# Kernel tuning notes

Measured on AMD Instinct MI355X. Metric: run time of the kernel, lower is better.

Reference implementation:

```python
import jax, jax.numpy as jnp
import numpy as np

TOKEN_SIZE = 4
NEIGHBOR_SIZE = 3


def setup_inputs() -> dict:
    key = jax.random.key(0)
    ks = jax.random.split(key, 8)
    B, C, H, W = 8, 256, 64, 64
    return {
        "blue_feat": jax.random.normal(ks[0], (B, C, H, W), jnp.float32),
        "white_feat": jax.random.normal(ks[1], (B, C, H, W), jnp.float32),
        "Wq": jax.random.normal(ks[2], (C, C), jnp.float32) * 0.05,
        "bq": jax.random.normal(ks[3], (C,), jnp.float32) * 0.05,
        "Wk": jax.random.normal(ks[4], (C, C), jnp.float32) * 0.05,
        "bk": jax.random.normal(ks[5], (C,), jnp.float32) * 0.05,
        "Wv": jax.random.normal(ks[6], (C, C), jnp.float32) * 0.05,
        "bv": jax.random.normal(ks[7], (C,), jnp.float32) * 0.05,
    }


def _tokens(x, nh, nw, ts):
    # [B,C,H,W] -> [B,nh,nw,C,ts*ts]
    B, C = x.shape[0], x.shape[1]
    return (x.reshape(B, C, nh, ts, nw, ts)
             .transpose(0, 2, 4, 1, 3, 5)
             .reshape(B, nh, nw, C, ts * ts))


def reference(blue_feat, white_feat, Wq, bq, Wk, bk, Wv, bv):
    ts, ns = TOKEN_SIZE, NEIGHBOR_SIZE
    pad = ns // 2
    B, C, H, W = blue_feat.shape
    scale = float((ts * ts) ** -0.5)

    # 1x1 conv projections (pointwise channel mix + bias)
    Q = jnp.einsum('bchw,oc->bohw', blue_feat, Wq) + bq[None, :, None, None]
    K = jnp.einsum('bchw,oc->bohw', white_feat, Wk) + bk[None, :, None, None]
    V = jnp.einsum('bchw,oc->bohw', white_feat, Wv) + bv[None, :, None, None]

    nh, nw = H // ts, W // ts  # H,W divisible by ts -> no padding branch
    Qt = _tokens(Q, nh, nw, ts)  # [B,nh,nw,C,D]
    Kt = _tokens(K, nh, nw, ts)
    Vt = _tokens(V, nh, nw, ts)

    # zero-padded token grid, gather 3x3 neighbor tokens (F.unfold equivalent)
    padw = ((0, 0), (pad, pad), (pad, pad), (0, 0), (0, 0))
    Kp = jnp.pad(Kt, padw)
    Vp = jnp.pad(Vt, padw)
    Knb = jnp.stack([Kp[:, di:di + nh, dj:dj + nw]
                     for di in range(ns) for dj in range(ns)], axis=3)  # [B,nh,nw,9,C,D]
    Vnb = jnp.stack([Vp[:, di:di + nh, dj:dj + nw]
                     for di in range(ns) for dj in range(ns)], axis=3)

    # per-channel attention over neighbor tokens
    attn = jax.nn.softmax(
        jnp.einsum('bhwcd,bhwncd->bhwcn', Qt, Knb) * scale, axis=-1)
    out = jnp.einsum('bhwcn,bhwncd->bhwcd', attn, Vnb)  # [B,nh,nw,C,D]

    enhanced = (out.reshape(B, nh, nw, C, ts, ts)
                   .transpose(0, 3, 1, 4, 2, 5)
                   .reshape(B, C, H, W))
    return blue_feat + enhanced  # out_proj is Identity since c1 == c2
```

## Files before the change

kernel.cpp:

```cpp
#include <hip/hip_runtime.h>
#include <hip/hip_bf16.h>
#include <stdint.h>

typedef float  f32x4  __attribute__((ext_vector_type(4)));
typedef float  f32x2  __attribute__((ext_vector_type(2)));
typedef __bf16 bf16x8 __attribute__((ext_vector_type(8)));


#define LROW 40

__global__ __launch_bounds__(256) void proj_gemm_kernel(
    const float* __restrict__ blue, const float* __restrict__ white,
    const float* __restrict__ Wq, const float* __restrict__ bq,
    const float* __restrict__ Wk, const float* __restrict__ bk,
    const float* __restrict__ Wv, const float* __restrict__ bv,
    __bf16* __restrict__ Qt, __bf16* __restrict__ Kt, __bf16* __restrict__ Vt)
{
  __shared__ __bf16 As[128 * LROW];
  __shared__ __bf16 Bs[128 * LROW];

  const int bidhw = blockIdx.x;
  const int lid   = (bidhw & 7) * 192 + (bidhw >> 3);
  const int nb    = lid / 6;
  const int bt    = lid % 6;
  const int tensor = (bt < 4) ? 1 + (bt & 1) : 0;
  const int ob     = (bt < 4) ? (bt >> 1) : (bt & 1);

  const float* X    = (tensor == 0) ? blue : white;
  const float* W    = (tensor == 0) ? Wq : (tensor == 1) ? Wk : Wv;
  const float* bias = (tensor == 0) ? bq : (tensor == 1) ? bk : bv;
  __bf16*      Out  = (tensor == 0) ? Qt : (tensor == 1) ? Kt : Vt;

  const int tid  = threadIdx.x;
  const int lane = tid & 63;
  const int wave = tid >> 6;
  const int wo   = wave >> 1;
  const int wn   = wave & 1;

  const int o0 = ob * 128;
  const int n0 = nb * 128;
  const int batch = n0 >> 12;
  const int p0    = n0 & 4095;
  const int tk0   = p0 >> 4;
  const int trow  = tk0 >> 4;
  const int tcol0 = tk0 & 15;

  const float* Xb = X + (size_t)batch * (256 * 4096);

  f32x4 acc[4][4];
#pragma unroll
  for (int i = 0; i < 4; ++i)
#pragma unroll
    for (int j = 0; j < 4; ++j) acc[i][j] = (f32x4)0.0f;

  const int arow  = tid >> 1;
  const int ahalf = tid & 1;
  const int n2   = tid & 63;
  const int ko   = tid >> 6;
  const int nloc = 2 * n2;
  const int tl   = nloc >> 4;
  const int d    = nloc & 15;
  const int hw   = (trow * 4 + (d >> 2)) * 64 + (tcol0 + tl) * 4 + (d & 3);

  const int lrow = lane & 15;
  const int lk   = (lane >> 4) * 8;

  for (int kk = 0; kk < 8; ++kk) {
    const int k0 = kk * 32;
    {
      const float* src = W + (size_t)(o0 + arow) * 256 + k0 + ahalf * 16;
      f32x4 t0 = *(const f32x4*)(src + 0);
      f32x4 t1 = *(const f32x4*)(src + 4);
      f32x4 t2 = *(const f32x4*)(src + 8);
      f32x4 t3 = *(const f32x4*)(src + 12);
      bf16x8 c0, c1;
#pragma unroll
      for (int q = 0; q < 4; ++q) { c0[q] = (__bf16)t0[q]; c0[q + 4] = (__bf16)t1[q]; }
#pragma unroll
      for (int q = 0; q < 4; ++q) { c1[q] = (__bf16)t2[q]; c1[q + 4] = (__bf16)t3[q]; }
      __bf16* dst = As + arow * LROW + ahalf * 16;
      *(bf16x8*)(dst + 0) = c0;
      *(bf16x8*)(dst + 8) = c1;
    }
    {
      const float* src = Xb + (size_t)(k0 + ko * 8) * 4096 + hw;
      f32x2 v0 = *(const f32x2*)(src + 0 * 4096);
      f32x2 v1 = *(const f32x2*)(src + 1 * 4096);
      f32x2 v2 = *(const f32x2*)(src + 2 * 4096);
      f32x2 v3 = *(const f32x2*)(src + 3 * 4096);
      f32x2 v4 = *(const f32x2*)(src + 4 * 4096);
      f32x2 v5 = *(const f32x2*)(src + 5 * 4096);
      f32x2 v6 = *(const f32x2*)(src + 6 * 4096);
      f32x2 v7 = *(const f32x2*)(src + 7 * 4096);
      bf16x8 r0, r1;
      r0[0] = (__bf16)v0[0]; r0[1] = (__bf16)v1[0]; r0[2] = (__bf16)v2[0]; r0[3] = (__bf16)v3[0];
      r0[4] = (__bf16)v4[0]; r0[5] = (__bf16)v5[0]; r0[6] = (__bf16)v6[0]; r0[7] = (__bf16)v7[0];
      r1[0] = (__bf16)v0[1]; r1[1] = (__bf16)v1[1]; r1[2] = (__bf16)v2[1]; r1[3] = (__bf16)v3[1];
      r1[4] = (__bf16)v4[1]; r1[5] = (__bf16)v5[1]; r1[6] = (__bf16)v6[1]; r1[7] = (__bf16)v7[1];
      *(bf16x8*)(Bs + (nloc + 0) * LROW + ko * 8) = r0;
      *(bf16x8*)(Bs + (nloc + 1) * LROW + ko * 8) = r1;
    }
    __syncthreads();

    bf16x8 a[4], b[4];
#pragma unroll
    for (int i = 0; i < 4; ++i)
      a[i] = *(const bf16x8*)(As + (wo * 64 + i * 16 + lrow) * LROW + lk);
#pragma unroll
    for (int j = 0; j < 4; ++j)
      b[j] = *(const bf16x8*)(Bs + (wn * 64 + j * 16 + lrow) * LROW + lk);
#pragma unroll
    for (int i = 0; i < 4; ++i)
#pragma unroll
      for (int j = 0; j < 4; ++j)
        acc[i][j] = __builtin_amdgcn_mfma_f32_16x16x32_bf16(a[i], b[j], acc[i][j], 0, 0, 0);
    __syncthreads();
  }

#pragma unroll
  for (int i = 0; i < 4; ++i) {
    const int obase = o0 + wo * 64 + i * 16 + (lane >> 4) * 4;
#pragma unroll
    for (int j = 0; j < 4; ++j) {
      const int n  = n0 + wn * 64 + j * 16 + (lane & 15);
      const int bb = n >> 12;
      const int p  = n & 4095;
      const int tt = p >> 4;
      const int tii = tt >> 4;
      const int tjj = tt & 15;
      const int dd  = p & 15;
      const size_t base = ((size_t)(bb * 16 + tii) * 256) * 256 + tjj * 16 + dd;
#pragma unroll
      for (int r = 0; r < 4; ++r) {
        const int o = obase + r;
        const float v = acc[i][j][r] + bias[o];
        Out[base + (size_t)o * 256] = (__bf16)v;
      }
    }
  }
}

__device__ __forceinline__ void unpack8(const uint4 v, float* f) {
  const uint32_t u0 = v.x, u1 = v.y, u2 = v.z, u3 = v.w;
  f[0] = __uint_as_float(u0 << 16); f[1] = __uint_as_float(u0 & 0xffff0000u);
  f[2] = __uint_as_float(u1 << 16); f[3] = __uint_as_float(u1 & 0xffff0000u);
  f[4] = __uint_as_float(u2 << 16); f[5] = __uint_as_float(u2 & 0xffff0000u);
  f[6] = __uint_as_float(u3 << 16); f[7] = __uint_as_float(u3 & 0xffff0000u);
}

__global__ __launch_bounds__(256) void attn_kernel(
    const __bf16* __restrict__ Qt, const __bf16* __restrict__ Kt,
    const __bf16* __restrict__ Vt, const float* __restrict__ blue,
    float* __restrict__ out)
{
  const int j   = blockIdx.x;
  const int bid = (j & 7) * 256 + (j >> 3);
  const int cg  = bid & 15;
  const int ti  = (bid >> 4) & 15;
  const int b   = bid >> 8;

  const int tid = threadIdx.x;
  const int tj  = tid & 15;
  const int cl  = tid >> 4;
  const int c   = cg * 16 + cl;

  float q[16];
  {
    const __bf16* p = Qt + ((((size_t)b * 16 + ti) * 256 + c) * 16 + tj) * 16;
    unpack8(*(const uint4*)p, q);
    unpack8(*(const uint4*)(p + 8), q + 8);
  }

  float s[9];
#pragma unroll
  for (int n = 0; n < 9; ++n) {
    const int yi = ti + n / 3 - 1;
    const int yj = tj + n % 3 - 1;
    float dot = 0.0f;
    if (yi >= 0 && yi < 16 && yj >= 0 && yj < 16) {
      const __bf16* p = Kt + ((((size_t)b * 16 + yi) * 256 + c) * 16 + yj) * 16;
      float kf[16];
      unpack8(*(const uint4*)p, kf);
      unpack8(*(const uint4*)(p + 8), kf + 8);
#pragma unroll
      for (int d = 0; d < 16; ++d) dot = fmaf(q[d], kf[d], dot);
    }
    s[n] = dot * 0.25f;
  }

  float m = s[0];
#pragma unroll
  for (int n = 1; n < 9; ++n) m = fmaxf(m, s[n]);
  float w[9], denom = 0.0f;
#pragma unroll
  for (int n = 0; n < 9; ++n) { w[n] = __expf(s[n] - m); denom += w[n]; }
  const float inv = 1.0f / denom;

  float o16[16];
#pragma unroll
  for (int d = 0; d < 16; ++d) o16[d] = 0.0f;
#pragma unroll
  for (int n = 0; n < 9; ++n) {
    const int yi = ti + n / 3 - 1;
    const int yj = tj + n % 3 - 1;
    if (yi >= 0 && yi < 16 && yj >= 0 && yj < 16) {
      const __bf16* p = Vt + ((((size_t)b * 16 + yi) * 256 + c) * 16 + yj) * 16;
      float vf[16];
      unpack8(*(const uint4*)p, vf);
      unpack8(*(const uint4*)(p + 8), vf + 8);
#pragma unroll
      for (int d = 0; d < 16; ++d) o16[d] = fmaf(w[n], vf[d], o16[d]);
    }
  }

  const size_t pbase = ((size_t)b * 256 + c) * 4096 + (size_t)(ti * 4) * 64 + tj * 4;
#pragma unroll
  for (int r = 0; r < 4; ++r) {
    f32x4 bl = *(const f32x4*)(blue + pbase + r * 64);
    f32x4 ov;
#pragma unroll
    for (int j2 = 0; j2 < 4; ++j2) ov[j2] = bl[j2] + o16[r * 4 + j2] * inv;
    *(f32x4*)(out + pbase + r * 64) = ov;
  }
}

extern "C" void kernel_launch(void* const* d_in, const int* in_sizes, int n_in,
                              void* d_out, int out_size, void* d_ws, size_t ws_size,
                              hipStream_t stream) {
  const float* blue  = (const float*)d_in[0];
  const float* white = (const float*)d_in[1];
  const float* Wq = (const float*)d_in[2];
  const float* bq = (const float*)d_in[3];
  const float* Wk = (const float*)d_in[4];
  const float* bk = (const float*)d_in[5];
  const float* Wv = (const float*)d_in[6];
  const float* bv = (const float*)d_in[7];
  float* out = (float*)d_out;

  const size_t tsz = (size_t)8 * 256 * 256 * 16;
  __bf16* Qt = (__bf16*)d_ws;
  __bf16* Kt = Qt + tsz;
  __bf16* Vt = Kt + tsz;

  proj_gemm_kernel<<<1536, 256, 0, stream>>>(blue, white, Wq, bq, Wk, bk, Wv, bv, Qt, Kt, Vt);
  attn_kernel<<<2048, 256, 0, stream>>>(Qt, Kt, Vt, blue, out);
}
```

Measured before the change: 72.70 us.

## Pre-convert weights to bf16 and compute two output tiles per GEMM block

Measured after the change: 76.17 us. +4.8%, slower.

```diff
diff --git a/kernel.cpp b/kernel.cpp
--- a/kernel.cpp
+++ b/kernel.cpp
@@ -6,8 +6,156 @@
 typedef float  f32x2  __attribute__((ext_vector_type(2)));
 typedef __bf16 bf16x8 __attribute__((ext_vector_type(8)));
 
-
 #define LROW 40
+
+__global__ __launch_bounds__(256) void wprep_kernel(
+    const float* __restrict__ Wq, const float* __restrict__ Wk,
+    const float* __restrict__ Wv, __bf16* __restrict__ Wbf)
+{
+  const int b = blockIdx.x;
+  const int t = b >> 5;
+  const float* src = (t == 0) ? Wq : (t == 1) ? Wk : Wv;
+  const int off = (b & 31) * 2048 + threadIdx.x * 8;
+  f32x4 v0 = *(const f32x4*)(src + off);
+  f32x4 v1 = *(const f32x4*)(src + off + 4);
+  bf16x8 r;
+#pragma unroll
+  for (int q = 0; q < 4; ++q) { r[q] = (__bf16)v0[q]; r[q + 4] = (__bf16)v1[q]; }
+  *(bf16x8*)(Wbf + t * 65536 + off) = r;
+}
+
+
+__global__ __launch_bounds__(256) void proj_gemm2_kernel(
+    const float* __restrict__ blue, const float* __restrict__ white,
+    const __bf16* __restrict__ Wbf,
+    const float* __restrict__ bq, const float* __restrict__ bk,
+    const float* __restrict__ bv,
+    __bf16* __restrict__ Qt, __bf16* __restrict__ Kt, __bf16* __restrict__ Vt)
+{
+  __shared__ __bf16 Bs[2][128 * LROW];
+
+  const int bidhw = blockIdx.x;
+  const int lid   = (bidhw & 7) * 96 + (bidhw >> 3);
+  const int nb    = lid / 3;
+  const int ty    = lid - nb * 3;
+
+  const float* X = (ty == 0) ? blue : white;
+  const __bf16 *W0, *W1; const float *bias0, *bias1;
+  __bf16 *Out0, *Out1; int oo0, oo1;
+  if (ty == 0)      { W0 = Wbf;                     W1 = Wbf + 128 * 256;
+                      bias0 = bq; bias1 = bq; Out0 = Qt; Out1 = Qt; oo0 = 0;   oo1 = 128; }
+  else if (ty == 1) { W0 = Wbf + 65536;             W1 = Wbf + 2 * 65536;
+                      bias0 = bk; bias1 = bv; Out0 = Kt; Out1 = Vt; oo0 = 0;   oo1 = 0;   }
+  else              { W0 = Wbf + 65536 + 128 * 256; W1 = Wbf + 2 * 65536 + 128 * 256;
+                      bias0 = bk; bias1 = bv; Out0 = Kt; Out1 = Vt; oo0 = 128; oo1 = 128; }
+
+  const int tid  = threadIdx.x;
+  const int lane = tid & 63;
+  const int wave = tid >> 6;
+  const int wo   = wave >> 1;
+  const int wn   = wave & 1;
+
+  const int n0    = nb * 128;
+  const int batch = n0 >> 12;
+  const int p0    = n0 & 4095;
+  const int tk0   = p0 >> 4;
+  const int trow  = tk0 >> 4;
+  const int tcol0 = tk0 & 15;
+  const float* Xb = X + (size_t)batch * (256 * 4096);
+
+  const int n2   = tid & 63;
+  const int ko   = tid >> 6;
+  const int nloc = 2 * n2;
+  const int tl   = nloc >> 4;
+  const int d    = nloc & 15;
+  const int hw   = (trow * 4 + (d >> 2)) * 64 + (tcol0 + tl) * 4 + (d & 3);
+  const float* srcB0 = Xb + (size_t)(ko * 8) * 4096 + hw;
+
+  f32x2 pre[8];
+#define LOADB(kk) { const float* s_ = srcB0 + (size_t)(kk) * 32 * 4096;            \
+    pre[0] = *(const f32x2*)(s_);         pre[1] = *(const f32x2*)(s_ + 4096);     \
+    pre[2] = *(const f32x2*)(s_ + 8192);  pre[3] = *(const f32x2*)(s_ + 12288);    \
+    pre[4] = *(const f32x2*)(s_ + 16384); pre[5] = *(const f32x2*)(s_ + 20480);    \
+    pre[6] = *(const f32x2*)(s_ + 24576); pre[7] = *(const f32x2*)(s_ + 28672); }
+
+  const int lrow = lane & 15;
+  const int lk   = (lane >> 4) * 8;
+  const int aoff = (wo * 64 + lrow) * 256 + lk;
+
+  f32x4 acc[2][4][4];
+#pragma unroll
+  for (int p = 0; p < 2; ++p)
+#pragma unroll
+    for (int i = 0; i < 4; ++i)
+#pragma unroll
+      for (int j = 0; j < 4; ++j) acc[p][i][j] = (f32x4)0.0f;
+
+  LOADB(0);
+
+  for (int kk = 0; kk < 8; ++kk) {
+    __bf16* bsw = &Bs[kk & 1][0];
+    bf16x8 r0, r1;
+#pragma unroll
+    for (int t = 0; t < 8; ++t) { r0[t] = (__bf16)pre[t][0]; r1[t] = (__bf16)pre[t][1]; }
+    *(bf16x8*)(bsw + (nloc + 0) * LROW + ko * 8) = r0;
+    *(bf16x8*)(bsw + (nloc + 1) * LROW + ko * 8) = r1;
+
+    bf16x8 af0[4], af1[4];
+#pragma unroll
+    for (int i = 0; i < 4; ++i) af0[i] = *(const bf16x8*)(W0 + aoff + i * 4096 + kk * 32);
+#pragma unroll
+    for (int i = 0; i < 4; ++i) af1[i] = *(const bf16x8*)(W1 + aoff + i * 4096 + kk * 32);
+
+    if (kk < 7) LOADB(kk + 1);
+
+    asm volatile("s_waitcnt lgkmcnt(0)" ::: "memory");
+    __builtin_amdgcn_s_barrier();
+    asm volatile("" ::: "memory");
+
+    const __bf16* bsr = &Bs[kk & 1][0];
+    bf16x8 bfrag[4];
+#pragma unroll
+    for (int j = 0; j < 4; ++j)
+      bfrag[j] = *(const bf16x8*)(bsr + (wn * 64 + j * 16 + lrow) * LROW + lk);
+#pragma unroll
+    for (int i = 0; i < 4; ++i)
+#pragma unroll
+      for (int j = 0; j < 4; ++j) {
+        acc[0][i][j] = __builtin_amdgcn_mfma_f32_16x16x32_bf16(af0[i], bfrag[j], acc[0][i][j], 0, 0, 0);
+        acc[1][i][j] = __builtin_amdgcn_mfma_f32_16x16x32_bf16(af1[i], bfrag[j], acc[1][i][j], 0, 0, 0);
+      }
+  }
+#undef LOADB
+
+#pragma unroll
+  for (int p = 0; p < 2; ++p) {
+    const __bf16* Wdummy = p ? W1 : W0; (void)Wdummy;
+    __bf16* Out = p ? Out1 : Out0;
+    const float* bias = p ? bias1 : bias0;
+    const int oo = p ? oo1 : oo0;
+#pragma unroll
+    for (int i = 0; i < 4; ++i) {
+      const int orow = wo * 64 + i * 16 + (lane >> 4) * 4;
+#pragma unroll
+      for (int j = 0; j < 4; ++j) {
+        const int n  = n0 + wn * 64 + j * 16 + (lane & 15);
+        const int bb = n >> 12;
+        const int pp = n & 4095;
+        const int tt = pp >> 4;
+        const int tii = tt >> 4;
+        const int tjj = tt & 15;
+        const int dd  = pp & 15;
+        const size_t base = ((size_t)(bb * 16 + tii) * 256) * 256 + tjj * 16 + dd;
+#pragma unroll
+        for (int r = 0; r < 4; ++r) {
+          const int o = oo + orow + r;
+          const float v = acc[p][i][j][r] + bias[o];
+          Out[base + (size_t)o * 256] = (__bf16)v;
+        }
+      }
+    }
+  }
+}
 
 __global__ __launch_bounds__(256) void proj_gemm_kernel(
     const float* __restrict__ blue, const float* __restrict__ white,
@@ -44,7 +192,6 @@
   const int tk0   = p0 >> 4;
   const int trow  = tk0 >> 4;
   const int tcol0 = tk0 & 15;
-
   const float* Xb = X + (size_t)batch * (256 * 4096);
 
   f32x4 acc[4][4];
@@ -183,7 +330,7 @@
       unpack8(*(const uint4*)p, kf);
       unpack8(*(const uint4*)(p + 8), kf + 8);
 #pragma unroll
-      for (int d = 0; d < 16; ++d) dot = fmaf(q[d], kf[d], dot);
+      for (int dd = 0; dd < 16; ++dd) dot = fmaf(q[dd], kf[dd], dot);
     }
     s[n] = dot * 0.25f;
   }
@@ -198,7 +345,7 @@
 
   float o16[16];
 #pragma unroll
-  for (int d = 0; d < 16; ++d) o16[d] = 0.0f;
+  for (int dd = 0; dd < 16; ++dd) o16[dd] = 0.0f;
 #pragma unroll
   for (int n = 0; n < 9; ++n) {
     const int yi = ti + n / 3 - 1;
@@ -209,7 +356,7 @@
       unpack8(*(const uint4*)p, vf);
       unpack8(*(const uint4*)(p + 8), vf + 8);
 #pragma unroll
-      for (int d = 0; d < 16; ++d) o16[d] = fmaf(w[n], vf[d], o16[d]);
+      for (int dd = 0; dd < 16; ++dd) o16[dd] = fmaf(w[n], vf[dd], o16[dd]);
     }
   }
 
@@ -242,6 +389,13 @@
   __bf16* Kt = Qt + tsz;
   __bf16* Vt = Kt + tsz;
 
-  proj_gemm_kernel<<<1536, 256, 0, stream>>>(blue, white, Wq, bq, Wk, bk, Wv, bv, Qt, Kt, Vt);
+  const size_t need = (3 * tsz + 3 * 65536) * sizeof(__bf16);
+  if (ws_size >= need) {
+    __bf16* Wbf = Vt + tsz;
+    wprep_kernel<<<96, 256, 0, stream>>>(Wq, Wk, Wv, Wbf);
+    proj_gemm2_kernel<<<768, 256, 0, stream>>>(blue, white, Wbf, bq, bk, bv, Qt, Kt, Vt);
+  } else {
+    proj_gemm_kernel<<<1536, 256, 0, stream>>>(blue, white, Wq, bq, Wk, bk, Wv, bv, Qt, Kt, Vt);
+  }
   attn_kernel<<<2048, 256, 0, stream>>>(Qt, Kt, Vt, blue, out);
 }
```

## Pre-convert inputs to bf16 channel-last and stream GEMM operands from global

Applied to the files above, without the earlier changes.

After: 99.60 us. 1.37x slower.

```diff
diff --git a/kernel.cpp b/kernel.cpp
--- a/kernel.cpp
+++ b/kernel.cpp
@@ -6,8 +6,152 @@
 typedef float  f32x2  __attribute__((ext_vector_type(2)));
 typedef __bf16 bf16x8 __attribute__((ext_vector_type(8)));
 
-
 #define LROW 40
+
+__global__ __launch_bounds__(256) void prep_kernel(
+    const float* __restrict__ blue, const float* __restrict__ white,
+    const float* __restrict__ Wq, const float* __restrict__ Wk,
+    const float* __restrict__ Wv,
+    __bf16* __restrict__ Xtb, __bf16* __restrict__ Xtw,
+    __bf16* __restrict__ Wbf)
+{
+  const int bid = blockIdx.x;
+  if (bid >= 1024) {
+    const int wb = bid - 1024;
+    const int t  = wb >> 5;
+    const float* src = (t == 0) ? Wq : (t == 1) ? Wk : Wv;
+    const int off = (wb & 31) * 2048 + threadIdx.x * 8;
+    f32x4 v0 = *(const f32x4*)(src + off);
+    f32x4 v1 = *(const f32x4*)(src + off + 4);
+    bf16x8 r;
+#pragma unroll
+    for (int q = 0; q < 4; ++q) { r[q] = (__bf16)v0[q]; r[q + 4] = (__bf16)v1[q]; }
+    *(bf16x8*)(Wbf + t * 65536 + off) = r;
+    return;
+  }
+  const int srcw = bid >> 9;
+  const int rem  = bid & 511;
+  const int b    = rem >> 6;
+  const int ti   = (rem >> 2) & 15;
+  const int cq   = rem & 3;
+  const float* X = srcw ? white : blue;
+  __bf16*     Xt = srcw ? Xtw : Xtb;
+
+  const int t  = threadIdx.x;
+  const int g  = t & 63;
+  const int cs = t >> 6;
+  const int c0 = cq * 64 + cs * 16;
+  const int hwb  = (ti * 4 + (g & 3)) * 64 + (g >> 2) * 4;
+  const int nimg = ti * 256 + (g >> 2) * 16 + (g & 3) * 4;
+  const float* Xb  = X + (size_t)b * (256 * 4096) + hwb;
+  __bf16*      dst = Xt + ((size_t)b * 4096 + nimg) * 256 + c0;
+
+#pragma unroll
+  for (int half = 0; half < 2; ++half) {
+    bf16x8 a0, a1, a2, a3;
+#pragma unroll
+    for (int i = 0; i < 8; ++i) {
+      const int c = c0 + half * 8 + i;
+      f32x4 v = *(const f32x4*)(Xb + (size_t)c * 4096);
+      a0[i] = (__bf16)v[0]; a1[i] = (__bf16)v[1];
+      a2[i] = (__bf16)v[2]; a3[i] = (__bf16)v[3];
+    }
+    *(bf16x8*)(dst + 0 * 256 + half * 8) = a0;
+    *(bf16x8*)(dst + 1 * 256 + half * 8) = a1;
+    *(bf16x8*)(dst + 2 * 256 + half * 8) = a2;
+    *(bf16x8*)(dst + 3 * 256 + half * 8) = a3;
+  }
+}
+
+__global__ __launch_bounds__(256, 3) void gemm_stream_kernel(
+    const __bf16* __restrict__ Xtb, const __bf16* __restrict__ Xtw,
+    const __bf16* __restrict__ Wbf,
+    const float* __restrict__ bq, const float* __restrict__ bk,
+    const float* __restrict__ bv,
+    __bf16* __restrict__ Qt, __bf16* __restrict__ Kt, __bf16* __restrict__ Vt)
+{
+  const int bid = blockIdx.x;
+  const int lid = (bid & 7) * 192 + (bid >> 3);
+  const int nb  = lid / 6;
+  const int bt  = lid % 6;
+  const int tensor = (bt < 4) ? 1 + (bt & 1) : 0;
+  const int ob     = (bt < 4) ? (bt >> 1) : (bt & 1);
+
+  const __bf16* Xt   = (tensor == 0) ? Xtb : Xtw;
+  const float*  bias = (tensor == 0) ? bq : (tensor == 1) ? bk : bv;
+  __bf16*       Out  = (tensor == 0) ? Qt : (tensor == 1) ? Kt : Vt;
+  const __bf16* Wp   = Wbf + tensor * 65536 + ob * 32768;
+
+  const int tid  = threadIdx.x;
+  const int lane = tid & 63;
+  const int wave = tid >> 6;
+  const int wo   = wave >> 1;
+  const int wn   = wave & 1;
+  const int lrow = lane & 15;
+  const int lk   = (lane >> 4) * 8;
+
+  const int o0 = ob * 128;
+  const int n0 = nb * 128;
+
+  const __bf16* abase = Wp + (size_t)(wo * 64 + lrow) * 256 + lk;
+  const __bf16* xbase = Xt + ((size_t)n0 + wn * 64 + lrow) * 256 + lk;
+
+  f32x4 acc[4][4];
+#pragma unroll
+  for (int i = 0; i < 4; ++i)
+#pragma unroll
+    for (int j = 0; j < 4; ++j) acc[i][j] = (f32x4)0.0f;
+
+  bf16x8 afA[4], bfA[4], afB[4], bfB[4];
+
+#define LOADF(AF, BF, kk) {                                                  \
+    _Pragma("unroll")                                                        \
+    for (int i = 0; i < 4; ++i)                                              \
+      AF[i] = *(const bf16x8*)(abase + (size_t)i * 16 * 256 + (kk) * 32);    \
+    _Pragma("unroll")                                                        \
+    for (int j = 0; j < 4; ++j)                                              \
+      BF[j] = *(const bf16x8*)(xbase + (size_t)j * 16 * 256 + (kk) * 32); }
+
+#define MFMAS(AF, BF) {                                                      \
+    _Pragma("unroll")                                                        \
+    for (int i = 0; i < 4; ++i)                                              \
+      _Pragma("unroll")                                                      \
+      for (int j = 0; j < 4; ++j)                                            \
+        acc[i][j] = __builtin_amdgcn_mfma_f32_16x16x32_bf16(AF[i], BF[j], acc[i][j], 0, 0, 0); }
+
+  LOADF(afA, bfA, 0);
+#pragma unroll
+  for (int kp = 0; kp < 4; ++kp) {
+    LOADF(afB, bfB, 2 * kp + 1);
+    MFMAS(afA, bfA);
+    if (kp < 3) LOADF(afA, bfA, 2 * kp + 2);
+    MFMAS(afB, bfB);
+  }
+#undef LOADF
+#undef MFMAS
+
+#pragma unroll
+  for (int i = 0; i < 4; ++i) {
+    const int obase = o0 + wo * 64 + i * 16 + (lane >> 4) * 4;
+#pragma unroll
+    for (int j = 0; j < 4; ++j) {
+      const int n  = n0 + wn * 64 + j * 16 + (lane & 15);
+      const int bb = n >> 12;
+      const int pp = n & 4095;
+      const int tt = pp >> 4;
+      const int tii = tt >> 4;
+      const int tjj = tt & 15;
+      const int dd  = pp & 15;
+      const size_t base = ((size_t)(bb * 16 + tii) * 256) * 256 + tjj * 16 + dd;
+#pragma unroll
+      for (int r = 0; r < 4; ++r) {
+        const int o = obase + r;
+        const float v = acc[i][j][r] + bias[o];
+        Out[base + (size_t)o * 256] = (__bf16)v;
+      }
+    }
+  }
+}
 
 __global__ __launch_bounds__(256) void proj_gemm_kernel(
     const float* __restrict__ blue, const float* __restrict__ white,
@@ -44,7 +188,6 @@
   const int tk0   = p0 >> 4;
   const int trow  = tk0 >> 4;
   const int tcol0 = tk0 & 15;
-
   const float* Xb = X + (size_t)batch * (256 * 4096);
 
   f32x4 acc[4][4];
@@ -183,7 +326,7 @@
       unpack8(*(const uint4*)p, kf);
       unpack8(*(const uint4*)(p + 8), kf + 8);
 #pragma unroll
-      for (int d = 0; d < 16; ++d) dot = fmaf(q[d], kf[d], dot);
+      for (int dd = 0; dd < 16; ++dd) dot = fmaf(q[dd], kf[dd], dot);
     }
     s[n] = dot * 0.25f;
   }
@@ -198,7 +341,7 @@
 
   float o16[16];
 #pragma unroll
-  for (int d = 0; d < 16; ++d) o16[d] = 0.0f;
+  for (int dd = 0; dd < 16; ++dd) o16[dd] = 0.0f;
 #pragma unroll
   for (int n = 0; n < 9; ++n) {
     const int yi = ti + n / 3 - 1;
@@ -209,7 +352,7 @@
       unpack8(*(const uint4*)p, vf);
       unpack8(*(const uint4*)(p + 8), vf + 8);
 #pragma unroll
-      for (int d = 0; d < 16; ++d) o16[d] = fmaf(w[n], vf[d], o16[d]);
+      for (int dd = 0; dd < 16; ++dd) o16[dd] = fmaf(w[n], vf[dd], o16[dd]);
     }
   }
 
@@ -238,10 +381,20 @@
   float* out = (float*)d_out;
 
   const size_t tsz = (size_t)8 * 256 * 256 * 16;
+  const size_t xsz = (size_t)8 * 4096 * 256;
   __bf16* Qt = (__bf16*)d_ws;
   __bf16* Kt = Qt + tsz;
   __bf16* Vt = Kt + tsz;
 
-  proj_gemm_kernel<<<1536, 256, 0, stream>>>(blue, white, Wq, bq, Wk, bk, Wv, bv, Qt, Kt, Vt);
+  const size_t need_new = (3 * tsz + 2 * xsz + 3 * 65536) * sizeof(__bf16);
+  if (ws_size >= need_new) {
+    __bf16* Xtb = Vt + tsz;
+    __bf16* Xtw = Xtb + xsz;
+    __bf16* Wbf = Xtw + xsz;
+    prep_kernel<<<1120, 256, 0, stream>>>(blue, white, Wq, Wk, Wv, Xtb, Xtw, Wbf);
+    gemm_stream_kernel<<<1536, 256, 0, stream>>>(Xtb, Xtw, Wbf, bq, bk, bv, Qt, Kt, Vt);
+  } else {
+    proj_gemm_kernel<<<1536, 256, 0, stream>>>(blue, white, Wq, bq, Wk, bk, Wv, bv, Qt, Kt, Vt);
+  }
   attn_kernel<<<2048, 256, 0, stream>>>(Qt, Kt, Vt, blue, out);
 }
```
